# Kernel optimization log

Hardware: AMD Instinct MI355X
Metric: run time of the kernel (lower is better)

## Reference

```python
import jax, jax.numpy as jnp
import numpy as np

B, NUM_ANCHORS, NUM_CLASSES = 32, 15130, 81
SCALE_XY, SCALE_WH = 0.1, 0.2
CRITERIA, MAX_OUT, SCORE_THRESH = 0.5, 200, 0.05


def setup_inputs() -> dict:
    key = jax.random.key(0)
    k1, k2, k3, k4 = jax.random.split(key, 4)
    ploc = jax.random.normal(k1, (B, 4, NUM_ANCHORS), dtype=jnp.float32)
    plabel = jax.random.normal(k2, (B, NUM_CLASSES, NUM_ANCHORS), dtype=jnp.float32)
    # default boxes in (cx, cy, w, h) form, all in [0, 1]
    xy = jax.random.uniform(k3, (NUM_ANCHORS, 2), dtype=jnp.float32, minval=0.05, maxval=0.95)
    wh = jax.random.uniform(k4, (NUM_ANCHORS, 2), dtype=jnp.float32, minval=0.02, maxval=0.3)
    dboxes_xywh = jnp.concatenate([xy, wh], axis=-1)
    return {"ploc": ploc, "plabel": plabel, "dboxes_xywh": dboxes_xywh}


def _iou(a, b):
    # a: [M,4] ltrb, b: [K,4] ltrb -> [M,K]
    lt = jnp.maximum(a[:, None, :2], b[None, :, :2])
    rb = jnp.minimum(a[:, None, 2:], b[None, :, 2:])
    wh = jnp.clip(rb - lt, 0.0)
    inter = wh[..., 0] * wh[..., 1]
    area_a = (a[:, 2] - a[:, 0]) * (a[:, 3] - a[:, 1])
    area_b = (b[:, 2] - b[:, 0]) * (b[:, 3] - b[:, 1])
    return inter / (area_a[:, None] + area_b[None, :] - inter + 1e-12)


def _decode(ploc, plabel, dboxes_xywh):
    # scale_back_batch: ploc [B,4,N] -> ltrb boxes [B,N,4]
    b = jnp.transpose(ploc, (0, 2, 1))
    xy = b[..., :2] * SCALE_XY * dboxes_xywh[:, 2:] + dboxes_xywh[:, :2]
    wh = jnp.exp(b[..., 2:] * SCALE_WH) * dboxes_xywh[:, 2:]
    ltrb = jnp.concatenate([xy - 0.5 * wh, xy + 0.5 * wh], axis=-1)  # [B,N,4]
    probs = jnp.transpose(jax.nn.softmax(plabel, axis=1), (0, 2, 1))  # [B,N,C]
    return ltrb, probs


def _nms_per_class(scores_c, boxes):
    # scores_c: [N], boxes: [N,4]
    s = jnp.where(scores_c > SCORE_THRESH, scores_c, 0.0)
    vals, idx = jax.lax.top_k(s, MAX_OUT)  # descending, matches score-sorted greedy order
    bx = boxes[idx]  # [MAX_OUT,4]
    iou = _iou(bx, bx)  # [MAX_OUT,MAX_OUT]
    later = jnp.arange(MAX_OUT)

    def body(i, keep):
        active = keep[i] & (vals[i] > 0.0)
        suppress = active & (iou[i] >= CRITERIA) & (later > i)
        return keep & ~suppress

    keep = jax.lax.fori_loop(0, MAX_OUT, body, jnp.ones((MAX_OUT,), bool))
    keep = keep & (vals > 0.0)
    return jnp.where(keep, vals, 0.0), bx


def _decode_single(probs_i, boxes_i):
    # skip background class 0
    cls_scores = probs_i[:, 1:].T  # [C-1, N]
    vals, bx = jax.vmap(_nms_per_class, in_axes=(0, None))(cls_scores, boxes_i)
    c1 = NUM_CLASSES - 1
    flat_v = vals.reshape(-1)                 # [(C-1)*MAX_OUT]
    flat_b = bx.reshape(-1, 4)
    labels = jnp.repeat(jnp.arange(1, c1 + 1, dtype=jnp.int32), MAX_OUT)
    top_v, top_i = jax.lax.top_k(flat_v, MAX_OUT)
    return flat_b[top_i], labels[top_i], top_v


def reference(ploc, plabel, dboxes_xywh):
    ltrb, probs = _decode(ploc, plabel, dboxes_xywh)
    boxes_out, labels_out, scores_out = jax.vmap(_decode_single)(probs, ltrb)
    return boxes_out, labels_out, scores_out
```

## Files before the change

kernel.cpp:

```cpp
#include <hip/hip_runtime.h>
#include <math.h>

namespace {
constexpr int BATCH = 32;
constexpr int NANCH = 15130;
constexpr int NCLS  = 81;
constexpr int C1    = 80;
constexpr int MAXO  = 200;
constexpr int APB   = 256;
constexpr int NBLKA = (NANCH + APB - 1) / APB;
constexpr int CAPK2 = 512;
constexpr int CAP   = 1024;
constexpr int CAPB  = 768;
constexpr int NBIN  = 2048;
constexpr int NBINK2 = 768;
constexpr unsigned BINBASE = 0x3D000000u;
constexpr int IMGCAP = C1 * MAXO;
}

#define SCORE_TH 0.05f
#define IOU_TH   0.5f

typedef unsigned long long u64;

__device__ __forceinline__ u64 shflx64(u64 v, int mask) {
    int lo = __shfl_xor((int)(unsigned)(v & 0xffffffffull), mask, 64);
    int hi = __shfl_xor((int)(unsigned)(v >> 32), mask, 64);
    return ((u64)(unsigned)hi << 32) | (unsigned)lo;
}

__device__ __forceinline__ void bitonic_desc(u64* keys, int P,
                                             int tid, int nthr) {
    for (int k = 2; k <= P; k <<= 1) {
        for (int j = k >> 1; j > 0; j >>= 1) {
            for (int i = tid; i < P; i += nthr) {
                int ixj = i ^ j;
                if (ixj > i) {
                    u64 a = keys[i], c = keys[ixj];
                    bool up = ((i & k) == 0);
                    if (up ? (a < c) : (a > c)) { keys[i] = c; keys[ixj] = a; }
                }
            }
            __syncthreads();
        }
    }
}

__device__ __forceinline__ u64 regsort256(u64 key, u64* lds, int tid) {
    for (int k = 2; k <= 256; k <<= 1) {
        for (int j = k >> 1; j > 0; j >>= 1) {
            u64 pv;
            if (j < 64) {
                pv = shflx64(key, j);
            } else {
                lds[tid] = key;
                __syncthreads();
                pv = lds[tid ^ j];
            }
            bool up = ((tid & k) == 0);
            bool lt = ((tid & j) == 0);
            u64 mx = (key > pv) ? key : pv;
            u64 mn = (key > pv) ? pv : key;
            key = (up == lt) ? mx : mn;
            if (j >= 64) __syncthreads();
        }
    }
    return key;
}

__device__ __forceinline__ void iou_parts(const float4 bb, const float aa,
                                          const float4 bi, const float ai,
                                          float& in_, float& dn) {
#pragma clang fp contract(off)
    float l = fmaxf(bi.x, bb.x);
    float t = fmaxf(bi.y, bb.y);
    float r = fminf(bi.z, bb.z);
    float d = fminf(bi.w, bb.w);
    in_ = fmaxf(r - l, 0.f) * fmaxf(d - t, 0.f);
    dn  = ai + aa - in_ + 1e-12f;
}

__global__ __launch_bounds__(256, 3) void ssd_decode_stats(
    const float* __restrict__ ploc, const float* __restrict__ plabel,
    const float* __restrict__ dboxes,
    float* __restrict__ ltrb, float* __restrict__ rowmax,
    float* __restrict__ rowsum,
    int* __restrict__ cntg, u64* __restrict__ bucket) {
#pragma clang fp contract(off)
    __shared__ int lcnt[C1], lbase[C1], lrank[C1];

    const int tid = threadIdx.x;
    const int b   = blockIdx.x / NBLKA;
    const int n0  = (blockIdx.x % NBLKA) * APB;
    const int n   = n0 + tid;
    const bool act = (n < NANCH);

    if (tid < C1) lcnt[tid] = 0;

    float x[NCLS];
    float s = 1.f;
    u64 w0 = 0, w1 = 0;
    if (act) {
        const float* pl = ploc + (size_t)b * 4 * NANCH + n;
        float px = pl[0], py = pl[NANCH], pw = pl[2 * NANCH],
              ph = pl[3 * NANCH];
        float4 db = reinterpret_cast<const float4*>(dboxes)[n];
        float cx = px * 0.1f * db.z + db.x;
        float cy = py * 0.1f * db.w + db.y;
        float w  = expf(pw * 0.2f) * db.z;
        float h  = expf(ph * 0.2f) * db.w;
        float4 o;
        o.x = cx - 0.5f * w; o.y = cy - 0.5f * h;
        o.z = cx + 0.5f * w; o.w = cy + 0.5f * h;
        reinterpret_cast<float4*>(ltrb)[(size_t)b * NANCH + n] = o;

        const float* pb = plabel + (size_t)b * NCLS * NANCH + n;
#pragma unroll
        for (int c = 0; c < NCLS; ++c) x[c] = pb[(size_t)c * NANCH];

        float m = -INFINITY;
#pragma unroll
        for (int c = 0; c < NCLS; ++c) m = fmaxf(m, x[c]);
#pragma unroll
        for (int c = 0; c < NCLS; ++c) x[c] = expf(x[c] - m);
        s = 0.f;
#pragma unroll
        for (int c = 0; c < NCLS; ++c) s += x[c];
        rowmax[(size_t)b * NANCH + n] = m;
        rowsum[(size_t)b * NANCH + n] = s;

        const float sc = s * SCORE_TH;
        const float lo = sc * 0.99999952f;
        const float hi = sc * 1.00000048f;
#pragma unroll
        for (int c = 1; c < NCLS; ++c) {
            float e = x[c];
            bool band = (e >= lo) && (e <= hi);
            bool pass = (e > hi);
            if (__any(band)) pass = band ? ((e / s) > SCORE_TH) : pass;
            if (pass) {
                atomicAdd(&lcnt[c - 1], 1);
                if (c <= 64) w0 |= 1ull << (c - 1);
                else         w1 |= 1ull << (c - 65);
            }
        }
    }
    __syncthreads();

    if (tid < C1) {
        int cn = lcnt[tid];
        lbase[tid] = (cn > 0) ? atomicAdd(&cntg[b * C1 + tid], cn) : 0;
        lrank[tid] = 0;
    }
    __syncthreads();

    if (act) {
#pragma unroll
        for (int c = 1; c < NCLS; ++c) {
            bool pass = (c <= 64) ? ((w0 >> (c - 1)) & 1ull)
                                  : ((w1 >> (c - 65)) & 1ull);
            if (pass) {
                int r = atomicAdd(&lrank[c - 1], 1);
                int pos = lbase[c - 1] + r;
                if (pos < CAPB) {
                    float p = x[c] / s;
                    bucket[(size_t)(b * C1 + (c - 1)) * CAPB + pos] =
                        ((u64)__float_as_uint(p) << 32)
                        | (u64)(0xFFFFFFFFu - (unsigned)n);
                }
            }
        }
    }
}

__global__ __launch_bounds__(256, 6) void ssd_class_nms(
    const float* __restrict__ plabel, const float* __restrict__ rowmax,
    const float* __restrict__ rowsum, const float* __restrict__ ltrb,
    const int* __restrict__ cntg, const u64* __restrict__ bucket,
    float* __restrict__ pcVals, float* __restrict__ pcBoxes,
    int* __restrict__ imgcnt, u64* __restrict__ imglist) {
    __shared__ u64 pool[MAXO * 4];
    __shared__ __align__(16) u64 candbox[CAPK2];
    __shared__ u64 nzsh[4];
    __shared__ int wtot[4];
    __shared__ int cnt, cutbin, fillcnt;

    unsigned* hist = (unsigned*)pool;
    u64* cand = candbox;
    float4* box4 = reinterpret_cast<float4*>(candbox);
    float* areas = reinterpret_cast<float*>(candbox) + 800;

    const int tid  = threadIdx.x;
    const int lane = tid & 63;
    const int wv   = tid >> 6;
    const int b    = blockIdx.x / C1;
    const int cls  = blockIdx.x % C1 + 1;
    const int bc   = b * C1 + (cls - 1);

    for (int i = tid; i < NBINK2; i += 256) hist[i] = 0u;
    if (tid == 0) { cnt = 0; cutbin = 1; fillcnt = 0; }
    if (tid < 4) nzsh[tid] = 0ull;
    __syncthreads();

    const float* pl = plabel + ((size_t)b * NCLS + cls) * NANCH;
    const float* rm = rowmax + (size_t)b * NANCH;
    const float* rs = rowsum + (size_t)b * NANCH;
    const u64* bkt = bucket + (size_t)bc * CAPB;

    const int gcount = cntg[bc];
    const bool ovf = (gcount > CAPB);
    int gathered;

    if (!ovf) {
        for (int i = tid; i < gcount; i += 256) {
            unsigned bits = (unsigned)(bkt[i] >> 32);
            unsigned bin = ((bits - BINBASE) >> 16) + 1u;
            if (bin > NBINK2 - 1) bin = NBINK2 - 1;
            atomicAdd(&hist[bin], 1u);
        }
        __syncthreads();

        const int base = tid * 3;
        int loc = (int)hist[base] + (int)hist[base + 1] + (int)hist[base + 2];
        int sfx = loc;
        for (int off = 1; off < 64; off <<= 1) {
            int t = __shfl_down(sfx, off, 64);
            if (lane + off < 64) sfx += t;
        }
        if (lane == 0) wtot[wv] = sfx;
        __syncthreads();
        int crossSuf = 0;
        for (int w2 = wv + 1; w2 < 4; ++w2) crossSuf += wtot[w2];
        const int nztot = wtot[0] + wtot[1] + wtot[2] + wtot[3];
        {
            int S = (sfx - loc) + crossSuf;
            for (int k = 2; k >= 0; --k) {
                int binv = (int)hist[base + k];
                int Sk = S + binv;
                int bin = base + k;
                if (bin >= 1 && Sk >= MAXO && S < MAXO) cutbin = bin;
                S = Sk;
            }
        }
        __syncthreads();
        const int B = (nztot >= MAXO) ? cutbin : 1;

        for (int i = tid; i < gcount; i += 256) {
            u64 k = bkt[i];
            unsigned bits = (unsigned)(k >> 32);
            unsigned bin = ((bits - BINBASE) >> 16) + 1u;
            if (bin > NBINK2 - 1) bin = NBINK2 - 1;
            if ((int)bin >= B) {
                int pos = atomicAdd(&cnt, 1);
                if (pos < CAPK2) cand[pos] = k;
            }
        }
        __syncthreads();
        gathered = min(cnt, CAPK2);
    } else {
        for (int n = tid; n < NANCH; n += 256) {
            float p = expf(pl[n] - rm[n]) / rs[n];
            if (p > SCORE_TH) {
                int pos = atomicAdd(&cnt, 1);
                if (pos < CAPK2)
                    cand[pos] = ((u64)__float_as_uint(p) << 32)
                              | (u64)(0xFFFFFFFFu - (unsigned)n);
            }
        }
        __syncthreads();
        gathered = min(cnt, CAPK2);
    }

    if (gathered <= 256) {
        u64 key = (tid < gathered) ? cand[tid] : 0ull;
        key = regsort256(key, cand, tid);
        __syncthreads();
        cand[tid] = key;
        if (tid < CAPK2 - 256) cand[256 + tid] = 0ull;
        __syncthreads();
    } else {
        for (int i = gathered + tid; i < CAPK2; i += 256) cand[i] = 0ull;
        __syncthreads();
        bitonic_desc(cand, CAPK2, tid, 256);
    }

    if (gathered < MAXO) {
        int* scanb = (int*)hist;
        const int need = MAXO - gathered;
        for (int base2 = 0; base2 < NANCH; base2 += 256) {
            if (fillcnt >= need) break;
            int n = base2 + tid;
            int flag = 0;
            if (n < NANCH) {
                float p = expf(pl[n] - rm[n]) / rs[n];
                flag = (p <= SCORE_TH) ? 1 : 0;
            }
            scanb[tid] = flag;
            __syncthreads();
            for (int off = 1; off < 256; off <<= 1) {
                int v  = scanb[tid];
                int vp = (tid >= off) ? scanb[tid - off] : 0;
                __syncthreads();
                scanb[tid] = v + vp;
                __syncthreads();
            }
            int excl = scanb[tid] - flag;
            if (flag && (fillcnt + excl) < need)
                cand[gathered + fillcnt + excl] =
                    (u64)(0xFFFFFFFFu - (unsigned)n);
            __syncthreads();
            if (tid == 0) fillcnt += scanb[255];
            __syncthreads();
        }
        __syncthreads();
    }

    u64 r0 = cand[lane], r1 = cand[64 + lane];
    u64 r2 = cand[128 + lane], r3 = cand[192 + lane];
    float4 b0, b1, b2, b3;
    float a0, a1, a2, a3, v0f, v1f, v2f, v3f;
    {
#pragma clang fp contract(off)
        const float4* lt4 = reinterpret_cast<const float4*>(ltrb)
                            + (size_t)b * NANCH;
        unsigned n0_ = 0xFFFFFFFFu - (unsigned)(r0 & 0xFFFFFFFFull);
        unsigned n1_ = 0xFFFFFFFFu - (unsigned)(r1 & 0xFFFFFFFFull);
        unsigned n2_ = 0xFFFFFFFFu - (unsigned)(r2 & 0xFFFFFFFFull);
        v0f = __uint_as_float((unsigned)(r0 >> 32));
        v1f = __uint_as_float((unsigned)(r1 >> 32));
        v2f = __uint_as_float((unsigned)(r2 >> 32));
        b0 = lt4[n0_]; b1 = lt4[n1_]; b2 = lt4[n2_];
        a0 = (b0.z - b0.x) * (b0.w - b0.y);
        a1 = (b1.z - b1.x) * (b1.w - b1.y);
        a2 = (b2.z - b2.x) * (b2.w - b2.y);
        if (lane < MAXO - 192) {
            unsigned n3_ = 0xFFFFFFFFu - (unsigned)(r3 & 0xFFFFFFFFull);
            v3f = __uint_as_float((unsigned)(r3 >> 32));
            b3 = lt4[n3_];
            a3 = (b3.z - b3.x) * (b3.w - b3.y);
        } else {
            v3f = 0.f; b3 = make_float4(0.f, 0.f, 0.f, 0.f); a3 = 0.f;
        }
    }
    __syncthreads();
    if (wv == 0) {
        box4[lane] = b0;        areas[lane] = a0;
        box4[64 + lane] = b1;   areas[64 + lane] = a1;
        box4[128 + lane] = b2;  areas[128 + lane] = a2;
        if (lane < MAXO - 192) { box4[192 + lane] = b3; areas[192 + lane] = a3; }
    }
    const bool j3v = (lane < MAXO - 192);
    const u64 vm0 = __ballot(v0f > 0.f);
    const u64 vm1 = __ballot(v1f > 0.f);
    const u64 vm2 = __ballot(v2f > 0.f);
    const u64 vm3 = __ballot(j3v && (v3f > 0.f));
    __syncthreads();

    u64* supflat = pool;

    u64 nz0 = 0, nz1 = 0, nz2 = 0, nz3 = 0;
    for (int i = wv; i < 64; i += 4) {
#pragma clang fp contract(off)
        float4 bi = box4[i]; float ai = areas[i];
        float i0, d0_, i1, d1_, i2, d2_, i3, d3_;
        iou_parts(b0, a0, bi, ai, i0, d0_);
        iou_parts(b1, a1, bi, ai, i1, d1_);
        iou_parts(b2, a2, bi, ai, i2, d2_);
        iou_parts(b3, a3, bi, ai, i3, d3_);
        float t0 = i0 + i0, t1 = i1 + i1, t2 = i2 + i2, t3 = i3 + i3;
        bool su0 = t0 >= d0_, su1 = t1 >= d1_, su2 = t2 >= d2_, su3 = t3 >= d3_;
        bool bd0 = !su0 && (t0 > d0_ * 0.99999952f);
        bool bd1 = !su1 && (t1 > d1_ * 0.99999952f);
        bool bd2 = !su2 && (t2 > d2_ * 0.99999952f);
        bool bd3 = !su3 && (t3 > d3_ * 0.99999952f);
        if (__any(bd0 | bd1 | bd2 | bd3)) {
            su0 = bd0 ? (i0 / d0_ >= IOU_TH) : su0;
            su1 = bd1 ? (i1 / d1_ >= IOU_TH) : su1;
            su2 = bd2 ? (i2 / d2_ >= IOU_TH) : su2;
            su3 = bd3 ? (i3 / d3_ >= IOU_TH) : su3;
        }
        u64 s0 = __ballot(su0 && (lane > i));
        u64 s1 = __ballot(su1);
        u64 s2 = __ballot(su2);
        u64 s3 = __ballot(su3 && j3v);
        if ((s0 | s1 | s2 | s3) != 0ull) {
            nz0 |= 1ull << i;
            if (lane == 0) {
                supflat[i * 4 + 0] = s0; supflat[i * 4 + 1] = s1;
                supflat[i * 4 + 2] = s2; supflat[i * 4 + 3] = s3;
            }
        }
    }
    for (int i = 64 + wv; i < 128; i += 4) {
#pragma clang fp contract(off)
        float4 bi = box4[i]; float ai = areas[i];
        float i1, d1_, i2, d2_, i3, d3_;
        iou_parts(b1, a1, bi, ai, i1, d1_);
        iou_parts(b2, a2, bi, ai, i2, d2_);
        iou_parts(b3, a3, bi, ai, i3, d3_);
        float t1 = i1 + i1, t2 = i2 + i2, t3 = i3 + i3;
        bool su1 = t1 >= d1_, su2 = t2 >= d2_, su3 = t3 >= d3_;
        bool bd1 = !su1 && (t1 > d1_ * 0.99999952f);
        bool bd2 = !su2 && (t2 > d2_ * 0.99999952f);
        bool bd3 = !su3 && (t3 > d3_ * 0.99999952f);
        if (__any(bd1 | bd2 | bd3)) {
            su1 = bd1 ? (i1 / d1_ >= IOU_TH) : su1;
            su2 = bd2 ? (i2 / d2_ >= IOU_TH) : su2;
            su3 = bd3 ? (i3 / d3_ >= IOU_TH) : su3;
        }
        u64 s1 = __ballot(su1 && (64 + lane > i));
        u64 s2 = __ballot(su2);
        u64 s3 = __ballot(su3 && j3v);
        if ((s1 | s2 | s3) != 0ull) {
            nz1 |= 1ull << (i - 64);
            if (lane == 0) {
                supflat[i * 4 + 1] = s1;
                supflat[i * 4 + 2] = s2; supflat[i * 4 + 3] = s3;
            }
        }
    }
    for (int i = 128 + wv; i < 192; i += 4) {
#pragma clang fp contract(off)
        float4 bi = box4[i]; float ai = areas[i];
        float i2, d2_, i3, d3_;
        iou_parts(b2, a2, bi, ai, i2, d2_);
        iou_parts(b3, a3, bi, ai, i3, d3_);
        float t2 = i2 + i2, t3 = i3 + i3;
        bool su2 = t2 >= d2_, su3 = t3 >= d3_;
        bool bd2 = !su2 && (t2 > d2_ * 0.99999952f);
        bool bd3 = !su3 && (t3 > d3_ * 0.99999952f);
        if (__any(bd2 | bd3)) {
            su2 = bd2 ? (i2 / d2_ >= IOU_TH) : su2;
            su3 = bd3 ? (i3 / d3_ >= IOU_TH) : su3;
        }
        u64 s2 = __ballot(su2 && (128 + lane > i));
        u64 s3 = __ballot(su3 && j3v);
        if ((s2 | s3) != 0ull) {
            nz2 |= 1ull << (i - 128);
            if (lane == 0) {
                supflat[i * 4 + 2] = s2; supflat[i * 4 + 3] = s3;
            }
        }
    }
    for (int i = 192 + wv; i < MAXO; i += 4) {
#pragma clang fp contract(off)
        float4 bi = box4[i]; float ai = areas[i];
        float i3, d3_;
        iou_parts(b3, a3, bi, ai, i3, d3_);
        float t3 = i3 + i3;
        bool su3 = t3 >= d3_;
        bool bd3 = !su3 && (t3 > d3_ * 0.99999952f);
        if (__any(bd3)) su3 = bd3 ? (i3 / d3_ >= IOU_TH) : su3;
        u64 s3 = __ballot(su3 && j3v && (192 + lane > i));
        if (s3 != 0ull) {
            nz3 |= 1ull << (i - 192);
            if (lane == 0) supflat[i * 4 + 3] = s3;
        }
    }
    if (lane == 0) {
        if (nz0) atomicOr(&nzsh[0], nz0);
        if (nz1) atomicOr(&nzsh[1], nz1);
        if (nz2) atomicOr(&nzsh[2], nz2);
        if (nz3) atomicOr(&nzsh[3], nz3);
    }
    __syncthreads();

    if (wv != 0) return;

    const u64 znz0 = nzsh[0], znz1 = nzsh[1], znz2 = nzsh[2], znz3 = nzsh[3];

    u64 k0 = ~0ull, k1 = ~0ull, k2 = ~0ull, k3 = ~0ull;
    {
        int i = -1;
        u64 c;
        if ((c = k0 & vm0 & znz0))      i = __builtin_ctzll(c);
        else if ((c = k1 & vm1 & znz1)) i = 64 + __builtin_ctzll(c);
        else if ((c = k2 & vm2 & znz2)) i = 128 + __builtin_ctzll(c);
        else if ((c = k3 & vm3 & znz3)) i = 192 + __builtin_ctzll(c);
        while (i >= 0) {
            int wr = i >> 6, bit = i & 63;
            if (wr == 0) {
                k0 &= ~supflat[i * 4 + 0]; k1 &= ~supflat[i * 4 + 1];
                k2 &= ~supflat[i * 4 + 2]; k3 &= ~supflat[i * 4 + 3];
            } else if (wr == 1) {
                k1 &= ~supflat[i * 4 + 1];
                k2 &= ~supflat[i * 4 + 2]; k3 &= ~supflat[i * 4 + 3];
            } else if (wr == 2) {
                k2 &= ~supflat[i * 4 + 2]; k3 &= ~supflat[i * 4 + 3];
            } else {
                k3 &= ~supflat[i * 4 + 3];
            }
            u64 above = (bit == 63) ? 0ull : (~0ull << (bit + 1));
            u64 cur = ((wr == 0) ? (k0 & vm0 & znz0)
                     : (wr == 1) ? (k1 & vm1 & znz1)
                     : (wr == 2) ? (k2 & vm2 & znz2)
                                 : (k3 & vm3 & znz3)) & above;
            i = -1;
            while (true) {
                if (cur) { i = wr * 64 + __builtin_ctzll(cur); break; }
                if (++wr >= 4) break;
                cur = (wr == 1) ? (k1 & vm1 & znz1)
                    : (wr == 2) ? (k2 & vm2 & znz2) : (k3 & vm3 & znz3);
            }
        }
    }

    {
        float* pv  = pcVals + (size_t)bc * MAXO;
        float4* pb4 = reinterpret_cast<float4*>(pcBoxes + (size_t)bc * MAXO * 4);
        bool kp0 = (k0 >> lane) & 1ull, kp1 = (k1 >> lane) & 1ull;
        bool kp2 = (k2 >> lane) & 1ull, kp3 = (k3 >> lane) & 1ull;
        pv[lane]        = (kp0 && v0f > 0.f) ? v0f : 0.f;
        pv[64 + lane]   = (kp1 && v1f > 0.f) ? v1f : 0.f;
        pv[128 + lane]  = (kp2 && v2f > 0.f) ? v2f : 0.f;
        pb4[lane] = b0; pb4[64 + lane] = b1; pb4[128 + lane] = b2;
        if (j3v) {
            pv[192 + lane] = (kp3 && v3f > 0.f) ? v3f : 0.f;
            pb4[192 + lane] = b3;
        }
    }

    {
        u64 km0 = k0 & vm0, km1 = k1 & vm1, km2 = k2 & vm2, km3 = k3 & vm3;
        int c0 = (int)__popcll(km0), c1 = (int)__popcll(km1);
        int c2 = (int)__popcll(km2), c3 = (int)__popcll(km3);
        int tot = c0 + c1 + c2 + c3;
        int kb = 0;
        if (lane == 0 && tot > 0) kb = atomicAdd(&imgcnt[b], tot);
        kb = __shfl(kb, 0);
        u64 below = (lane == 0) ? 0ull : (~0ull >> (64 - lane));
        u64* dst = imglist + (size_t)b * IMGCAP + kb;
        const u64 himask = 0xFFFFFFFF00000000ull;
        if ((km0 >> lane) & 1ull) {
            unsigned g = (unsigned)((cls - 1) * MAXO + lane);
            dst[__popcll(km0 & below)] =
                (r0 & himask) | (u64)(0xFFFFFFFFu - g);
        }
        if ((km1 >> lane) & 1ull) {
            unsigned g = (unsigned)((cls - 1) * MAXO + 64 + lane);
            dst[c0 + __popcll(km1 & below)] =
                (r1 & himask) | (u64)(0xFFFFFFFFu - g);
        }
        if ((km2 >> lane) & 1ull) {
            unsigned g = (unsigned)((cls - 1) * MAXO + 128 + lane);
            dst[c0 + c1 + __popcll(km2 & below)] =
                (r2 & himask) | (u64)(0xFFFFFFFFu - g);
        }
        if ((km3 >> lane) & 1ull) {
            unsigned g = (unsigned)((cls - 1) * MAXO + 192 + lane);
            dst[c0 + c1 + c2 + __popcll(km3 & below)] =
                (r3 & himask) | (u64)(0xFFFFFFFFu - g);
        }
    }
}

__global__ __launch_bounds__(256) void ssd_final_topk(
    const float* __restrict__ pcVals, const float* __restrict__ pcBoxes,
    const int* __restrict__ imgcnt, const u64* __restrict__ imglist,
    float* __restrict__ out) {
    __shared__ unsigned int hist[NBIN];
    __shared__ u64 cand[CAP];
    __shared__ int wtot[4];
    __shared__ int cnt, cutbin, nztot;

    const int tid  = threadIdx.x;
    const int lane = tid & 63;
    const int wv   = tid >> 6;
    const int b    = blockIdx.x;
    const int TOT  = C1 * MAXO;
    const float* pv = pcVals + (size_t)b * TOT;
    const int NZ   = imgcnt[b];

    for (int i = tid; i < NBIN; i += 256) hist[i] = 0u;
    if (tid == 0) { cnt = 0; cutbin = 1; }
    __syncthreads();

    int count;
    if (NZ >= MAXO) {
        const u64* lst = imglist + (size_t)b * IMGCAP;
        for (int i = tid; i < NZ; i += 256) {
            unsigned bits = (unsigned)(lst[i] >> 32);
            unsigned bin = ((bits - BINBASE) >> 15) + 1u;
            if (bin > NBIN - 1) bin = NBIN - 1;
            atomicAdd(&hist[bin], 1u);
        }
        __syncthreads();

        const int base = tid * 8;
        int loc = 0;
        for (int k = 0; k < 8; ++k) loc += (int)hist[base + k];
        int sfx = loc;
        for (int off = 1; off < 64; off <<= 1) {
            int t = __shfl_down(sfx, off, 64);
            if (lane + off < 64) sfx += t;
        }
        if (lane == 0) wtot[wv] = sfx;
        __syncthreads();
        int crossSuf = 0;
        for (int w2 = wv + 1; w2 < 4; ++w2) crossSuf += wtot[w2];
        {
            int S = (sfx - loc) + crossSuf;
            for (int k = 7; k >= 0; --k) {
                int binv = (int)hist[base + k];
                int Sk = S + binv;
                int bin = base + k;
                if (bin >= 1 && Sk >= MAXO && S < MAXO) cutbin = bin;
                S = Sk;
            }
        }
        __syncthreads();
        const int B = cutbin;

        for (int i = tid; i < NZ; i += 256) {
            u64 k = lst[i];
            unsigned bits = (unsigned)(k >> 32);
            unsigned bin = ((bits - BINBASE) >> 15) + 1u;
            if (bin > NBIN - 1) bin = NBIN - 1;
            if ((int)bin >= B) {
                int pos = atomicAdd(&cnt, 1);
                if (pos < CAP) cand[pos] = k;
            }
        }
        __syncthreads();
        count = min(cnt, CAP);
    } else {
        for (int g = tid; g < TOT; g += 256) {
            float v = pv[g];
            if (v > 0.f) {
                unsigned bits = __float_as_uint(v);
                unsigned bin = ((bits - BINBASE) >> 15) + 1u;
                if (bin > NBIN - 1) bin = NBIN - 1;
                atomicAdd(&hist[bin], 1u);
            }
        }
        __syncthreads();
        const int base = tid * 8;
        int loc = 0;
        for (int k = 0; k < 8; ++k) loc += (int)hist[base + k];
        int sfx = loc;
        for (int off = 1; off < 64; off <<= 1) {
            int t = __shfl_down(sfx, off, 64);
            if (lane + off < 64) sfx += t;
        }
        if (lane == 0) wtot[wv] = sfx;
        __syncthreads();
        int crossSuf = 0;
        for (int w2 = wv + 1; w2 < 4; ++w2) crossSuf += wtot[w2];
        if (tid == 0) nztot = wtot[0] + wtot[1] + wtot[2] + wtot[3];
        {
            int S = (sfx - loc) + crossSuf;
            for (int k = 7; k >= 0; --k) {
                int binv = (int)hist[base + k];
                int Sk = S + binv;
                int bin = base + k;
                if (bin >= 1 && Sk >= MAXO && S < MAXO) cutbin = bin;
                S = Sk;
            }
        }
        __syncthreads();
        int B = (nztot >= MAXO) ? cutbin : 1;

        for (int g = tid; g < TOT; g += 256) {
            float v = pv[g];
            if (v > 0.f) {
                unsigned bits = __float_as_uint(v);
                unsigned bin = ((bits - BINBASE) >> 15) + 1u;
                if (bin > NBIN - 1) bin = NBIN - 1;
                if ((int)bin >= B) {
                    int pos = atomicAdd(&cnt, 1);
                    if (pos < CAP)
                        cand[pos] = ((u64)bits << 32)
                                  | (u64)(0xFFFFFFFFu - (unsigned)g);
                }
            }
        }
        __syncthreads();
        count = min(cnt, CAP);

        if (count < MAXO) {
            if (tid == 0) {
                int c = count;
                for (int g = 0; g < TOT && c < MAXO; ++g) {
                    if (!(pv[g] > 0.f)) {
                        cand[c++] = (u64)(0xFFFFFFFFu - (unsigned)g);
                    }
                }
                cnt = c;
            }
            __syncthreads();
            count = min(cnt, CAP);
        }
    }

    u64 key;
    if (count <= 256) {
        key = (tid < count) ? cand[tid] : 0ull;
        key = regsort256(key, cand, tid);
    } else {
        int P = 256; while (P < count) P <<= 1;
        for (int i = count + tid; i < P; i += 256) cand[i] = 0ull;
        __syncthreads();
        bitonic_desc(cand, P, tid, 256);
        key = cand[tid];
    }

    if (tid < MAXO) {
        float sc      = __uint_as_float((unsigned)(key >> 32));
        unsigned flat = 0xFFFFFFFFu - (unsigned)(key & 0xFFFFFFFFull);
        int cls = (int)(flat / MAXO) + 1;
        const float4 bb =
            reinterpret_cast<const float4*>(pcBoxes)[(size_t)b * TOT + flat];
        reinterpret_cast<float4*>(out)[(size_t)b * MAXO + tid] = bb;
        out[(size_t)BATCH * MAXO * 4 + (size_t)b * MAXO + tid] = (float)cls;
        out[(size_t)BATCH * MAXO * 5 + (size_t)b * MAXO + tid] = sc;
    }
}

extern "C" void kernel_launch(void* const* d_in, const int* in_sizes, int n_in,
                              void* d_out, int out_size, void* d_ws,
                              size_t ws_size, hipStream_t stream) {
    const float* ploc   = (const float*)d_in[0];
    const float* plabel = (const float*)d_in[1];
    const float* dboxes = (const float*)d_in[2];
    float* out = (float*)d_out;

    float* ws      = (float*)d_ws;
    float* ltrb    = ws;
    float* rowmax  = ltrb   + (size_t)BATCH * NANCH * 4;
    float* rowsum  = rowmax + (size_t)BATCH * NANCH;
    float* pcVals  = rowsum + (size_t)BATCH * NANCH;
    float* pcBoxes = pcVals + (size_t)BATCH * C1 * MAXO;
    int*   cntg    = (int*)(pcBoxes + (size_t)BATCH * C1 * MAXO * 4);
    int*   imgcnt  = cntg + BATCH * C1;
    char*  after   = (char*)(imgcnt + BATCH);
    u64* bucket = (u64*)(after + ((16 - (((size_t)after) & 15)) & 15));
    u64* imglist = bucket + (size_t)BATCH * C1 * CAPB;

    hipMemsetAsync(cntg, 0, (size_t)(BATCH * C1 + BATCH) * sizeof(int), stream);
    ssd_decode_stats<<<BATCH * NBLKA, APB, 0, stream>>>(
        ploc, plabel, dboxes, ltrb, rowmax, rowsum, cntg, bucket);
    ssd_class_nms<<<BATCH * C1, 256, 0, stream>>>(
        plabel, rowmax, rowsum, ltrb, cntg, bucket, pcVals, pcBoxes,
        imgcnt, imglist);
    ssd_final_topk<<<BATCH, 256, 0, stream>>>(
        pcVals, pcBoxes, imgcnt, imglist, out);
}
```

Before: 194.1 us.

## Drop per-thread logit array in decode kernel, re-read logits to raise occupancy

Removes the 81-entry per-thread register array in the decode/softmax kernel. Logits are re-read from global memory in several passes (max, sum of exps, threshold test, bucket write), and the launch bound rises from 3 to 6 blocks per SM. The threshold test now compares the log-space difference against log(s*thresh), calling exp only near the boundary, and threads with no passing classes skip the second loop. This cuts register pressure and exp count in exchange for up to three extra reads of plabel, which may hit cache, plus a changed near-threshold decision path that could alter rounding at the boundary.

```diff
diff --git a/kernel.cpp b/kernel.cpp
--- a/kernel.cpp
+++ b/kernel.cpp
@@ -80,7 +80,7 @@
     dn  = ai + aa - in_ + 1e-12f;
 }
 
-__global__ __launch_bounds__(256, 3) void ssd_decode_stats(
+__global__ __launch_bounds__(256, 6) void ssd_decode_stats(
     const float* __restrict__ ploc, const float* __restrict__ plabel,
     const float* __restrict__ dboxes,
     float* __restrict__ ltrb, float* __restrict__ rowmax,
@@ -97,9 +97,9 @@
 
     if (tid < C1) lcnt[tid] = 0;
 
-    float x[NCLS];
-    float s = 1.f;
+    float m = -INFINITY, s = 1.f;
     u64 w0 = 0, w1 = 0;
+    const float* pb = plabel + (size_t)b * NCLS * NANCH + (act ? n : 0);
     if (act) {
         const float* pl = ploc + (size_t)b * 4 * NANCH + n;
         float px = pl[0], py = pl[NANCH], pw = pl[2 * NANCH],
@@ -114,30 +114,31 @@
         o.z = cx + 0.5f * w; o.w = cy + 0.5f * h;
         reinterpret_cast<float4*>(ltrb)[(size_t)b * NANCH + n] = o;
 
-        const float* pb = plabel + (size_t)b * NCLS * NANCH + n;
 #pragma unroll
-        for (int c = 0; c < NCLS; ++c) x[c] = pb[(size_t)c * NANCH];
-
-        float m = -INFINITY;
-#pragma unroll
-        for (int c = 0; c < NCLS; ++c) m = fmaxf(m, x[c]);
-#pragma unroll
-        for (int c = 0; c < NCLS; ++c) x[c] = expf(x[c] - m);
+        for (int c = 0; c < NCLS; ++c) m = fmaxf(m, pb[(size_t)c * NANCH]);
         s = 0.f;
 #pragma unroll
-        for (int c = 0; c < NCLS; ++c) s += x[c];
+        for (int c = 0; c < NCLS; ++c) s += expf(pb[(size_t)c * NANCH] - m);
         rowmax[(size_t)b * NANCH + n] = m;
         rowsum[(size_t)b * NANCH + n] = s;
 
         const float sc = s * SCORE_TH;
         const float lo = sc * 0.99999952f;
         const float hi = sc * 1.00000048f;
+        const float Lt = logf(sc);
 #pragma unroll
         for (int c = 1; c < NCLS; ++c) {
-            float e = x[c];
-            bool band = (e >= lo) && (e <= hi);
-            bool pass = (e > hi);
-            if (__any(band)) pass = band ? ((e / s) > SCORE_TH) : pass;
+            float d = pb[(size_t)c * NANCH] - m;
+            bool pass;
+            if (d > Lt + 1e-4f) {
+                pass = true;
+            } else if (d < Lt - 1e-4f) {
+                pass = false;
+            } else {
+                float e = expf(d);
+                pass = (e > hi);
+                if (e >= lo && e <= hi) pass = ((e / s) > SCORE_TH);
+            }
             if (pass) {
                 atomicAdd(&lcnt[c - 1], 1);
                 if (c <= 64) w0 |= 1ull << (c - 1);
@@ -154,7 +155,7 @@
     }
     __syncthreads();
 
-    if (act) {
+    if (act && (w0 | w1)) {
 #pragma unroll
         for (int c = 1; c < NCLS; ++c) {
             bool pass = (c <= 64) ? ((w0 >> (c - 1)) & 1ull)
@@ -163,7 +164,7 @@
                 int r = atomicAdd(&lrank[c - 1], 1);
                 int pos = lbase[c - 1] + r;
                 if (pos < CAPB) {
-                    float p = x[c] / s;
+                    float p = expf(pb[(size_t)c * NANCH] - m) / s;
                     bucket[(size_t)(b * C1 + (c - 1)) * CAPB + pos] =
                         ((u64)__float_as_uint(p) << 32)
                         | (u64)(0xFFFFFFFFu - (unsigned)n);
```

After: 374.5 us. 1.93x slower.
